# Performance work log

Measured on AMD Instinct MI355X. Metric: run time of the kernel, lower is better.

## Reference

```python
import jax, jax.numpy as jnp
import numpy as np

B, S, D, H = 4, 2048, 1024, 16
DH = D // H


def setup_inputs() -> dict:
    key = jax.random.key(0)
    k1, k2, k3, k4, k5 = jax.random.split(key, 5)
    X = jax.random.normal(k1, (B, S, D), dtype=jnp.float32)
    W1 = jax.random.normal(k2, (3 * D, D), dtype=jnp.float32) * 0.02
    b1 = jax.random.normal(k3, (3 * D,), dtype=jnp.float32) * 0.01
    W2 = jax.random.normal(k4, (D, D), dtype=jnp.float32) * 0.02
    b2 = jax.random.normal(k5, (D,), dtype=jnp.float32) * 0.01
    return {"X": X, "W1": W1, "b1": b1, "W2": W2, "b2": b2}


def reference(X, W1, b1, W2, b2):
    b, s, d = X.shape
    # fused QKV projection (nn.Linear: y = x @ W.T + b)
    Y = X @ W1.T + b1                                   # [B,S,3D]
    Q, K, V = jnp.split(Y, 3, axis=2)                   # each [B,S,D]
    # reshape(x): view (B,S,H,DH) then permute(0,2,3,1) -> [B,H,DH,S]
    q = Q.reshape(b, s, H, DH).transpose(0, 2, 3, 1)    # [B,H,DH,S]
    v = V.reshape(b, s, H, DH).transpose(0, 2, 3, 1)    # [B,H,DH,S]
    # reshape(x, k=True): permute(0,2,1,3) -> [B,H,S,DH]
    k = K.reshape(b, s, H, DH).transpose(0, 2, 1, 3)    # [B,H,S,DH]
    # w = q @ k / sqrt(q.size(-1)) ; note q.size(-1) == S in this layout
    w = jnp.einsum('bhds,bhse->bhde', q, k) / jnp.sqrt(jnp.asarray(s, X.dtype))  # [B,H,DH,DH]
    w = jax.nn.softmax(w, axis=-1)
    out = jnp.einsum('bhde,bhes->bhds', w, v)           # [B,H,DH,S]
    # cat(): raw contiguous view of [B,H,DH,S] into [B,S,H*DH] (memory-order reshape)
    out = out.reshape(b, s, H * DH)                     # [B,S,D]
    return out @ W2.T + b2
```

## Files before the change

### kernel.cpp

```cpp
#include <hip/hip_runtime.h>
#include <stdint.h>

#define B_ 4
#define S_ 2048
#define D_ 1024
#define H_ 16
#define DH_ 64
#define M_TOT (B_*S_)
#define N1_ (3*D_)
#define K_ D_
#define NCH 8

typedef __bf16 bf16_8 __attribute__((ext_vector_type(8)));
typedef float  f32x4  __attribute__((ext_vector_type(4)));

typedef __attribute__((address_space(1))) const void* gas_t;
typedef __attribute__((address_space(3))) void*       las_t;

__device__ __forceinline__ unsigned short f2bf(float f) {
    union { float f; unsigned u; } v; v.f = f;
    unsigned r = v.u + 0x7FFFu + ((v.u >> 16) & 1u);
    return (unsigned short)(r >> 16);
}

__device__ __forceinline__ void async_ld16(const void* g, void* l) {
    __builtin_amdgcn_global_load_lds((gas_t)g, (las_t)l, 16, 0, 0);
}

__global__ __launch_bounds__(256)
void cast_kernel(const float* __restrict__ X, const float* __restrict__ W1,
                 const float* __restrict__ W2, unsigned short* __restrict__ Xb,
                 unsigned short* __restrict__ W1b, unsigned short* __restrict__ W2b) {
    const int nX  = (M_TOT * K_) / 4;
    const int nW1 = (N1_ * K_) / 4;
    int i = blockIdx.x * 256 + threadIdx.x;
    const float4* src; unsigned short* dst; int j;
    if (i < nX)            { src = (const float4*)X;  dst = Xb;  j = i; }
    else if (i < nX + nW1) { src = (const float4*)W1; dst = W1b; j = i - nX; }
    else                   { src = (const float4*)W2; dst = W2b; j = i - nX - nW1; }
    float4 v = src[j];
    ushort4 o;
    o.x = f2bf(v.x); o.y = f2bf(v.y); o.z = f2bf(v.z); o.w = f2bf(v.w);
    ((ushort4*)dst)[j] = o;
}

template<int N, bool OUT_BF16>
__global__ __launch_bounds__(256)
void gemm_bt(const unsigned short* __restrict__ A,
             const unsigned short* __restrict__ Bm,
             const float* __restrict__ bias,
             void* __restrict__ C, int K) {
    __shared__ unsigned short As[128 * 64];
    __shared__ unsigned short Bs[128 * 64];
    const int t    = threadIdx.x;
    const int wid  = t >> 6;
    const int lane = t & 63;
    const int lrow = lane & 15;
    const int lq   = lane >> 4;
    const int m0   = blockIdx.y * 128;
    const int n0   = blockIdx.x * 128;
    const int wm   = (wid >> 1) * 64;
    const int wn   = (wid & 1) * 64;

    f32x4 acc[4][4] = {};

    for (int k0 = 0; k0 < K; k0 += 64) {
#pragma unroll
        for (int p = 0; p < 4; p++) {
            const int c   = p * 256 + t;
            const int row = c >> 3;
            const int kb  = (c & 7) ^ (row & 7);
            async_ld16(A  + (size_t)(m0 + row) * K + k0 + kb * 8, (char*)As + c * 16);
            async_ld16(Bm + (size_t)(n0 + row) * K + k0 + kb * 8, (char*)Bs + c * 16);
        }
        __syncthreads();

#pragma unroll
        for (int ks = 0; ks < 2; ks++) {
            bf16_8 af[4], bfr[4];
#pragma unroll
            for (int mt = 0; mt < 4; mt++) {
                const int r  = wm + mt * 16 + lrow;
                const int kb = (ks * 4 + lq) ^ (r & 7);
                af[mt] = *(const bf16_8*)(As + (r * 8 + kb) * 8);
            }
#pragma unroll
            for (int nt = 0; nt < 4; nt++) {
                const int r  = wn + nt * 16 + lrow;
                const int kb = (ks * 4 + lq) ^ (r & 7);
                bfr[nt] = *(const bf16_8*)(Bs + (r * 8 + kb) * 8);
            }
#pragma unroll
            for (int mt = 0; mt < 4; mt++)
#pragma unroll
                for (int nt = 0; nt < 4; nt++)
                    acc[mt][nt] = __builtin_amdgcn_mfma_f32_16x16x32_bf16(af[mt], bfr[nt], acc[mt][nt], 0, 0, 0);
        }
        __syncthreads();
    }

#pragma unroll
    for (int nt = 0; nt < 4; nt++) {
        const int col = n0 + wn + nt * 16 + lrow;
        const float bv = bias[col];
#pragma unroll
        for (int mt = 0; mt < 4; mt++) {
            const int row = m0 + wm + mt * 16 + lq * 4;
            f32x4 a = acc[mt][nt];
            if (OUT_BF16) {
                unsigned short* Cp = (unsigned short*)C;
#pragma unroll
                for (int i = 0; i < 4; i++)
                    Cp[(size_t)(row + i) * N + col] = f2bf(a[i] + bv);
            } else {
                float* Cp = (float*)C;
#pragma unroll
                for (int i = 0; i < 4; i++)
                    Cp[(size_t)(row + i) * N + col] = a[i] + bv;
            }
        }
    }
}

__global__ __launch_bounds__(256)
void attn_scores(const unsigned short* __restrict__ Y, float* __restrict__ Scp) {
    __shared__ unsigned short Qs[64 * 72];
    __shared__ unsigned short Ks[64 * 72];
    const int bh = blockIdx.x, ch = blockIdx.y;
    const int b = bh >> 4, h = bh & 15;
    const size_t ybase = (size_t)b * S_ * 3072;
    const int qoff = h * 64, koff = D_ + h * 64;
    const int t = threadIdx.x, wid = t >> 6, lane = t & 63;
    const int lrow = lane & 15, lq = lane >> 4;

    f32x4 acc[4] = {};
    const int sbeg = ch * (S_ / NCH);
    for (int s0 = sbeg; s0 < sbeg + S_ / NCH; s0 += 64) {
#pragma unroll
        for (int p = 0; p < 4; p++) {
            int idx = p * 256 + t;
            int r = idx >> 4, cg = (idx & 15) * 4;
            const size_t gb = ybase + (size_t)(s0 + r) * 3072;
            ushort4 q4 = *(const ushort4*)(Y + gb + qoff + cg);
            ushort4 k4 = *(const ushort4*)(Y + gb + koff + cg);
            Qs[(cg + 0) * 72 + r] = q4.x; Qs[(cg + 1) * 72 + r] = q4.y;
            Qs[(cg + 2) * 72 + r] = q4.z; Qs[(cg + 3) * 72 + r] = q4.w;
            Ks[(cg + 0) * 72 + r] = k4.x; Ks[(cg + 1) * 72 + r] = k4.y;
            Ks[(cg + 2) * 72 + r] = k4.z; Ks[(cg + 3) * 72 + r] = k4.w;
        }
        __syncthreads();
#pragma unroll
        for (int ks = 0; ks < 2; ks++) {
            bf16_8 aq = *(const bf16_8*)(Qs + (wid * 16 + lrow) * 72 + ks * 32 + lq * 8);
#pragma unroll
            for (int nt = 0; nt < 4; nt++) {
                bf16_8 bk = *(const bf16_8*)(Ks + (nt * 16 + lrow) * 72 + ks * 32 + lq * 8);
                acc[nt] = __builtin_amdgcn_mfma_f32_16x16x32_bf16(aq, bk, acc[nt], 0, 0, 0);
            }
        }
        __syncthreads();
    }

    float* out = Scp + (size_t)(bh * NCH + ch) * 64 * 64;
#pragma unroll
    for (int nt = 0; nt < 4; nt++)
#pragma unroll
        for (int i = 0; i < 4; i++)
            out[(wid * 16 + lq * 4 + i) * 64 + nt * 16 + lrow] = acc[nt][i];
}

__global__ __launch_bounds__(256)
void attn_softmax(const float* __restrict__ Scp, unsigned short* __restrict__ Wb) {
    const int bh = blockIdx.x;
    const int t = threadIdx.x;
    const int d = t >> 2, q = t & 3;
    float s[16] = {};
#pragma unroll
    for (int c = 0; c < NCH; c++) {
        const float4* p = (const float4*)(Scp + ((size_t)(bh * NCH + c) * 64 + d) * 64 + q * 16);
#pragma unroll
        for (int j = 0; j < 4; j++) {
            float4 v = p[j];
            s[j*4+0] += v.x; s[j*4+1] += v.y; s[j*4+2] += v.z; s[j*4+3] += v.w;
        }
    }
    const float scale = 0.022097086912079608f;
    float m = -3.0e38f;
#pragma unroll
    for (int i = 0; i < 16; i++) { s[i] *= scale; m = fmaxf(m, s[i]); }
    m = fmaxf(m, __shfl_xor(m, 1));
    m = fmaxf(m, __shfl_xor(m, 2));
    float sum = 0.f;
#pragma unroll
    for (int i = 0; i < 16; i++) { s[i] = __expf(s[i] - m); sum += s[i]; }
    sum += __shfl_xor(sum, 1);
    sum += __shfl_xor(sum, 2);
    const float inv = 1.0f / sum;
    unsigned short* w = Wb + (size_t)bh * 4096 + d * 64 + q * 16;
    ushort4 o0, o1, o2, o3;
    o0.x=f2bf(s[0]*inv);  o0.y=f2bf(s[1]*inv);  o0.z=f2bf(s[2]*inv);  o0.w=f2bf(s[3]*inv);
    o1.x=f2bf(s[4]*inv);  o1.y=f2bf(s[5]*inv);  o1.z=f2bf(s[6]*inv);  o1.w=f2bf(s[7]*inv);
    o2.x=f2bf(s[8]*inv);  o2.y=f2bf(s[9]*inv);  o2.z=f2bf(s[10]*inv); o2.w=f2bf(s[11]*inv);
    o3.x=f2bf(s[12]*inv); o3.y=f2bf(s[13]*inv); o3.z=f2bf(s[14]*inv); o3.w=f2bf(s[15]*inv);
    ((ushort4*)w)[0]=o0; ((ushort4*)w)[1]=o1; ((ushort4*)w)[2]=o2; ((ushort4*)w)[3]=o3;
}

__global__ __launch_bounds__(256)
void attn_out(const unsigned short* __restrict__ Y, const unsigned short* __restrict__ Wb,
              unsigned short* __restrict__ O) {
    __shared__ unsigned short Ws[64 * 72];
    const int bh = blockIdx.x, sc = blockIdx.y;
    const int b = bh >> 4, h = bh & 15;
    const size_t ybase = (size_t)b * S_ * 3072;
    const int voff = 2 * D_ + h * 64;
    const int t = threadIdx.x, wid = t >> 6, lane = t & 63;
    const int lrow = lane & 15, lq = lane >> 4;

    {
        const int d = t >> 2, q = t & 3;
        const uint4* src = (const uint4*)(Wb + (size_t)bh * 4096 + d * 64 + q * 16);
        uint4* dst = (uint4*)(Ws + d * 72 + q * 16);
        dst[0] = src[0];
        *(uint4*)(Ws + d * 72 + q * 16 + 8) = src[1];
    }
    __syncthreads();

    bf16_8 aw[4][2];
#pragma unroll
    for (int mt = 0; mt < 4; mt++)
#pragma unroll
        for (int ks = 0; ks < 2; ks++)
            aw[mt][ks] = *(const bf16_8*)(Ws + (mt * 16 + lrow) * 72 + ks * 32 + lq * 8);

    const size_t obase = (size_t)b * (H_ * DH_ * S_) + (size_t)h * (DH_ * S_);
    const int s0 = sc * 256 + wid * 64;
    f32x4 o[4][4] = {};
#pragma unroll
    for (int ks = 0; ks < 2; ks++) {
        bf16_8 bv[4];
#pragma unroll
        for (int nt = 0; nt < 4; nt++)
            bv[nt] = *(const bf16_8*)(Y + ybase + (size_t)(s0 + nt * 16 + lrow) * 3072 + voff + ks * 32 + lq * 8);
#pragma unroll
        for (int mt = 0; mt < 4; mt++)
#pragma unroll
            for (int nt = 0; nt < 4; nt++)
                o[mt][nt] = __builtin_amdgcn_mfma_f32_16x16x32_bf16(aw[mt][ks], bv[nt], o[mt][nt], 0, 0, 0);
    }
#pragma unroll
    for (int mt = 0; mt < 4; mt++)
#pragma unroll
        for (int nt = 0; nt < 4; nt++) {
            const int d = mt * 16 + lq * 4;
            const int s = s0 + nt * 16 + lrow;
#pragma unroll
            for (int i = 0; i < 4; i++)
                O[obase + (size_t)(d + i) * S_ + s] = f2bf(o[mt][nt][i]);
        }
}

extern "C" void kernel_launch(void* const* d_in, const int* in_sizes, int n_in,
                              void* d_out, int out_size, void* d_ws, size_t ws_size,
                              hipStream_t stream) {
    const float* X  = (const float*)d_in[0];
    const float* W1 = (const float*)d_in[1];
    const float* b1 = (const float*)d_in[2];
    const float* W2 = (const float*)d_in[3];
    const float* b2 = (const float*)d_in[4];

    char* ws = (char*)d_ws;
    unsigned short* Xb  = (unsigned short*)(ws + 0);
    unsigned short* W1b = (unsigned short*)(ws + (16u << 20));
    unsigned short* W2b = (unsigned short*)(ws + (22u << 20));
    unsigned short* Yb  = (unsigned short*)(ws + (24u << 20));
    unsigned short* Wb  = (unsigned short*)(ws + 0);
    unsigned short* Ob  = (unsigned short*)(ws + (1u << 20));
    float* Scp = (float*)d_out;

    cast_kernel<<<12288, 256, 0, stream>>>(X, W1, W2, Xb, W1b, W2b);
    gemm_bt<N1_, true><<<dim3(N1_ / 128, M_TOT / 128), 256, 0, stream>>>(Xb, W1b, b1, Yb, K_);
    attn_scores<<<dim3(64, NCH), 256, 0, stream>>>(Yb, Scp);
    attn_softmax<<<64, 256, 0, stream>>>(Scp, Wb);
    attn_out<<<dim3(64, NCH), 256, 0, stream>>>(Yb, Wb, Ob);
    gemm_bt<D_, false><<<dim3(D_ / 128, M_TOT / 128), 256, 0, stream>>>(Ob, W2b, b2, d_out, K_);
}
```

Measured before the change: 212.3 us.

## Emit transposed Q/K from QKV GEMM epilogue and async-load them in scores

The QKV projection now has its own epilogue that writes Q and K in a head-major, sequence-contiguous [B,H,DH,S] layout and V as a separate [B,S,D] buffer. The scores kernel no longer transposes element by element through LDS. It loads tiles with async global-to-LDS copies and an XOR swizzle. The sequence split for the scores kernel is doubled to raise parallelism, while attn_out keeps its old split. In exchange the GEMM epilogue does strided transposed stores, and the softmax must reduce twice as many partials.

```diff
diff --git a/kernel.cpp b/kernel.cpp
--- a/kernel.cpp
+++ b/kernel.cpp
@@ -9,7 +9,8 @@
 #define M_TOT (B_*S_)
 #define N1_ (3*D_)
 #define K_ D_
-#define NCH 8
+#define NCH 16
+#define SCH 8
 
 typedef __bf16 bf16_8 __attribute__((ext_vector_type(8)));
 typedef float  f32x4  __attribute__((ext_vector_type(4)));
@@ -44,12 +45,12 @@
     ((ushort4*)dst)[j] = o;
 }
 
-template<int N, bool OUT_BF16>
-__global__ __launch_bounds__(256)
-void gemm_bt(const unsigned short* __restrict__ A,
-             const unsigned short* __restrict__ Bm,
-             const float* __restrict__ bias,
-             void* __restrict__ C, int K) {
+__global__ __launch_bounds__(256)
+void gemm_qkv(const unsigned short* __restrict__ A,
+              const unsigned short* __restrict__ Bm,
+              const float* __restrict__ bias,
+              unsigned short* __restrict__ Qt, unsigned short* __restrict__ Kt,
+              unsigned short* __restrict__ Vb) {
     __shared__ unsigned short As[128 * 64];
     __shared__ unsigned short Bs[128 * 64];
     const int t    = threadIdx.x;
@@ -64,6 +65,97 @@
 
     f32x4 acc[4][4] = {};
 
+    for (int k0 = 0; k0 < K_; k0 += 64) {
+#pragma unroll
+        for (int p = 0; p < 4; p++) {
+            const int c   = p * 256 + t;
+            const int row = c >> 3;
+            const int kb  = (c & 7) ^ (row & 7);
+            async_ld16(A  + (size_t)(m0 + row) * K_ + k0 + kb * 8, (char*)As + c * 16);
+            async_ld16(Bm + (size_t)(n0 + row) * K_ + k0 + kb * 8, (char*)Bs + c * 16);
+        }
+        __syncthreads();
+#pragma unroll
+        for (int ks = 0; ks < 2; ks++) {
+            bf16_8 af[4], bfr[4];
+#pragma unroll
+            for (int mt = 0; mt < 4; mt++) {
+                const int r  = wm + mt * 16 + lrow;
+                const int kb = (ks * 4 + lq) ^ (r & 7);
+                af[mt] = *(const bf16_8*)(As + (r * 8 + kb) * 8);
+            }
+#pragma unroll
+            for (int nt = 0; nt < 4; nt++) {
+                const int r  = wn + nt * 16 + lrow;
+                const int kb = (ks * 4 + lq) ^ (r & 7);
+                bfr[nt] = *(const bf16_8*)(Bs + (r * 8 + kb) * 8);
+            }
+#pragma unroll
+            for (int mt = 0; mt < 4; mt++)
+#pragma unroll
+                for (int nt = 0; nt < 4; nt++)
+                    acc[mt][nt] = __builtin_amdgcn_mfma_f32_16x16x32_bf16(af[mt], bfr[nt], acc[mt][nt], 0, 0, 0);
+        }
+        __syncthreads();
+    }
+
+    const int third = n0 >> 10;
+    if (third < 2) {
+        unsigned short* T = third ? Kt : Qt;
+#pragma unroll
+        for (int nt = 0; nt < 4; nt++) {
+            const int gcol = n0 + wn + nt * 16 + lrow;
+            const float bv = bias[gcol];
+            const int col  = gcol & 1023;
+            const int hh = col >> 6, d = col & 63;
+#pragma unroll
+            for (int mt = 0; mt < 4; mt++) {
+                const int row = m0 + wm + mt * 16 + lq * 4;
+                const int bb = row >> 11, s = row & 2047;
+                f32x4 a = acc[mt][nt];
+                ushort4 o;
+                o.x = f2bf(a[0] + bv); o.y = f2bf(a[1] + bv);
+                o.z = f2bf(a[2] + bv); o.w = f2bf(a[3] + bv);
+                *(ushort4*)(T + ((size_t)((bb * 16 + hh) * 64 + d)) * 2048 + s) = o;
+            }
+        }
+    } else {
+#pragma unroll
+        for (int nt = 0; nt < 4; nt++) {
+            const int gcol = n0 + wn + nt * 16 + lrow;
+            const float bv = bias[gcol];
+            const int col  = gcol & 1023;
+#pragma unroll
+            for (int mt = 0; mt < 4; mt++) {
+                const int row = m0 + wm + mt * 16 + lq * 4;
+                f32x4 a = acc[mt][nt];
+#pragma unroll
+                for (int i = 0; i < 4; i++)
+                    Vb[(size_t)(row + i) * 1024 + col] = f2bf(a[i] + bv);
+            }
+        }
+    }
+}
+
+__global__ __launch_bounds__(256)
+void gemm_bt(const unsigned short* __restrict__ A,
+             const unsigned short* __restrict__ Bm,
+             const float* __restrict__ bias,
+             float* __restrict__ C, int K, int N) {
+    __shared__ unsigned short As[128 * 64];
+    __shared__ unsigned short Bs[128 * 64];
+    const int t    = threadIdx.x;
+    const int wid  = t >> 6;
+    const int lane = t & 63;
+    const int lrow = lane & 15;
+    const int lq   = lane >> 4;
+    const int m0   = blockIdx.y * 128;
+    const int n0   = blockIdx.x * 128;
+    const int wm   = (wid >> 1) * 64;
+    const int wn   = (wid & 1) * 64;
+
+    f32x4 acc[4][4] = {};
+
     for (int k0 = 0; k0 < K; k0 += 64) {
 #pragma unroll
         for (int p = 0; p < 4; p++) {
@@ -74,7 +166,6 @@
             async_ld16(Bm + (size_t)(n0 + row) * K + k0 + kb * 8, (char*)Bs + c * 16);
         }
         __syncthreads();
-
 #pragma unroll
         for (int ks = 0; ks < 2; ks++) {
             bf16_8 af[4], bfr[4];
@@ -107,54 +198,47 @@
         for (int mt = 0; mt < 4; mt++) {
             const int row = m0 + wm + mt * 16 + lq * 4;
             f32x4 a = acc[mt][nt];
-            if (OUT_BF16) {
-                unsigned short* Cp = (unsigned short*)C;
-#pragma unroll
-                for (int i = 0; i < 4; i++)
-                    Cp[(size_t)(row + i) * N + col] = f2bf(a[i] + bv);
-            } else {
-                float* Cp = (float*)C;
-#pragma unroll
-                for (int i = 0; i < 4; i++)
-                    Cp[(size_t)(row + i) * N + col] = a[i] + bv;
-            }
-        }
-    }
-}
-
-__global__ __launch_bounds__(256)
-void attn_scores(const unsigned short* __restrict__ Y, float* __restrict__ Scp) {
-    __shared__ unsigned short Qs[64 * 72];
-    __shared__ unsigned short Ks[64 * 72];
+#pragma unroll
+            for (int i = 0; i < 4; i++)
+                C[(size_t)(row + i) * N + col] = a[i] + bv;
+        }
+    }
+}
+
+__global__ __launch_bounds__(256)
+void attn_scores(const unsigned short* __restrict__ Qt,
+                 const unsigned short* __restrict__ Kt,
+                 float* __restrict__ Scp) {
+    __shared__ unsigned short Qs[64 * 64];
+    __shared__ unsigned short Ks[64 * 64];
     const int bh = blockIdx.x, ch = blockIdx.y;
-    const int b = bh >> 4, h = bh & 15;
-    const size_t ybase = (size_t)b * S_ * 3072;
-    const int qoff = h * 64, koff = D_ + h * 64;
     const int t = threadIdx.x, wid = t >> 6, lane = t & 63;
     const int lrow = lane & 15, lq = lane >> 4;
+    const size_t qb = (size_t)bh * 64 * 2048;
+    const int kbase = ch * (S_ / NCH);
 
     f32x4 acc[4] = {};
-    const int sbeg = ch * (S_ / NCH);
-    for (int s0 = sbeg; s0 < sbeg + S_ / NCH; s0 += 64) {
-#pragma unroll
-        for (int p = 0; p < 4; p++) {
-            int idx = p * 256 + t;
-            int r = idx >> 4, cg = (idx & 15) * 4;
-            const size_t gb = ybase + (size_t)(s0 + r) * 3072;
-            ushort4 q4 = *(const ushort4*)(Y + gb + qoff + cg);
-            ushort4 k4 = *(const ushort4*)(Y + gb + koff + cg);
-            Qs[(cg + 0) * 72 + r] = q4.x; Qs[(cg + 1) * 72 + r] = q4.y;
-            Qs[(cg + 2) * 72 + r] = q4.z; Qs[(cg + 3) * 72 + r] = q4.w;
-            Ks[(cg + 0) * 72 + r] = k4.x; Ks[(cg + 1) * 72 + r] = k4.y;
-            Ks[(cg + 2) * 72 + r] = k4.z; Ks[(cg + 3) * 72 + r] = k4.w;
+    for (int k0 = 0; k0 < S_ / NCH; k0 += 64) {
+#pragma unroll
+        for (int p = 0; p < 2; p++) {
+            const int c   = p * 256 + t;
+            const int row = c >> 3;
+            const int kb  = (c & 7) ^ (row & 7);
+            const size_t off = qb + (size_t)row * 2048 + kbase + k0 + kb * 8;
+            async_ld16(Qt + off, (char*)Qs + c * 16);
+            async_ld16(Kt + off, (char*)Ks + c * 16);
         }
         __syncthreads();
 #pragma unroll
         for (int ks = 0; ks < 2; ks++) {
-            bf16_8 aq = *(const bf16_8*)(Qs + (wid * 16 + lrow) * 72 + ks * 32 + lq * 8);
+            const int rA  = wid * 16 + lrow;
+            const int kbA = (ks * 4 + lq) ^ (rA & 7);
+            bf16_8 aq = *(const bf16_8*)(Qs + (rA * 8 + kbA) * 8);
 #pragma unroll
             for (int nt = 0; nt < 4; nt++) {
-                bf16_8 bk = *(const bf16_8*)(Ks + (nt * 16 + lrow) * 72 + ks * 32 + lq * 8);
+                const int rB  = nt * 16 + lrow;
+                const int kbB = (ks * 4 + lq) ^ (rB & 7);
+                bf16_8 bk = *(const bf16_8*)(Ks + (rB * 8 + kbB) * 8);
                 acc[nt] = __builtin_amdgcn_mfma_f32_16x16x32_bf16(aq, bk, acc[nt], 0, 0, 0);
             }
         }
@@ -206,13 +290,12 @@
 }
 
 __global__ __launch_bounds__(256)
-void attn_out(const unsigned short* __restrict__ Y, const unsigned short* __restrict__ Wb,
+void attn_out(const unsigned short* __restrict__ Vb, const unsigned short* __restrict__ Wb,
               unsigned short* __restrict__ O) {
     __shared__ unsigned short Ws[64 * 72];
     const int bh = blockIdx.x, sc = blockIdx.y;
     const int b = bh >> 4, h = bh & 15;
-    const size_t ybase = (size_t)b * S_ * 3072;
-    const int voff = 2 * D_ + h * 64;
+    const int voff = h * 64;
     const int t = threadIdx.x, wid = t >> 6, lane = t & 63;
     const int lrow = lane & 15, lq = lane >> 4;
 
@@ -232,6 +315,7 @@
         for (int ks = 0; ks < 2; ks++)
             aw[mt][ks] = *(const bf16_8*)(Ws + (mt * 16 + lrow) * 72 + ks * 32 + lq * 8);
 
+    const size_t vbase = (size_t)b * S_ * 1024;
     const size_t obase = (size_t)b * (H_ * DH_ * S_) + (size_t)h * (DH_ * S_);
     const int s0 = sc * 256 + wid * 64;
     f32x4 o[4][4] = {};
@@ -240,7 +324,7 @@
         bf16_8 bv[4];
 #pragma unroll
         for (int nt = 0; nt < 4; nt++)
-            bv[nt] = *(const bf16_8*)(Y + ybase + (size_t)(s0 + nt * 16 + lrow) * 3072 + voff + ks * 32 + lq * 8);
+            bv[nt] = *(const bf16_8*)(Vb + vbase + (size_t)(s0 + nt * 16 + lrow) * 1024 + voff + ks * 32 + lq * 8);
 #pragma unroll
         for (int mt = 0; mt < 4; mt++)
 #pragma unroll
@@ -272,15 +356,17 @@
     unsigned short* Xb  = (unsigned short*)(ws + 0);
     unsigned short* W1b = (unsigned short*)(ws + (16u << 20));
     unsigned short* W2b = (unsigned short*)(ws + (22u << 20));
-    unsigned short* Yb  = (unsigned short*)(ws + (24u << 20));
+    unsigned short* Qt  = (unsigned short*)(ws + (24u << 20));
+    unsigned short* Kt  = (unsigned short*)(ws + (40u << 20));
+    unsigned short* Vb  = (unsigned short*)(ws + (56u << 20));
     unsigned short* Wb  = (unsigned short*)(ws + 0);
     unsigned short* Ob  = (unsigned short*)(ws + (1u << 20));
     float* Scp = (float*)d_out;
 
     cast_kernel<<<12288, 256, 0, stream>>>(X, W1, W2, Xb, W1b, W2b);
-    gemm_bt<N1_, true><<<dim3(N1_ / 128, M_TOT / 128), 256, 0, stream>>>(Xb, W1b, b1, Yb, K_);
-    attn_scores<<<dim3(64, NCH), 256, 0, stream>>>(Yb, Scp);
+    gemm_qkv<<<dim3(N1_ / 128, M_TOT / 128), 256, 0, stream>>>(Xb, W1b, b1, Qt, Kt, Vb);
+    attn_scores<<<dim3(64, NCH), 256, 0, stream>>>(Qt, Kt, Scp);
     attn_softmax<<<64, 256, 0, stream>>>(Scp, Wb);
-    attn_out<<<dim3(64, NCH), 256, 0, stream>>>(Yb, Wb, Ob);
-    gemm_bt<D_, false><<<dim3(D_ / 128, M_TOT / 128), 256, 0, stream>>>(Ob, W2b, b2, d_out, K_);
-}
+    attn_out<<<dim3(64, SCH), 256, 0, stream>>>(Vb, Wb, Ob);
+    gemm_bt<<<dim3(D_ / 128, M_TOT / 128), 256, 0, stream>>>(Ob, W2b, b2, (float*)d_out, K_, D_);
+}
```

Result: slower. 265.6 us (+25.1%).
